# Kernel optimization log

Measured on AMD Instinct MI355X. Metric: run time of the kernel, lower is better.

The kernel has to match this reference:

```python
import jax, jax.numpy as jnp
import numpy as np

H = 16
D_MODEL = 1024
D_K = D_MODEL // H
NEG = -1e9


def setup_inputs() -> dict:
    key = jax.random.key(0)
    ks = jax.random.split(key, 12)
    B, S = 2, 2048
    inp = {
        "query": jax.random.normal(ks[0], (B, S, D_MODEL), jnp.float32),
        "key": jax.random.normal(ks[1], (B, S, D_MODEL), jnp.float32),
        "value": jax.random.normal(ks[2], (B, S, D_MODEL), jnp.float32),
        "mask": jnp.ones((B, 1, S), jnp.int32),
    }
    s = 1.0 / np.sqrt(D_MODEL)
    for i, nm in enumerate(["Wq", "Wk", "Wv", "Wo"]):
        inp[nm] = jax.random.normal(ks[3 + i], (D_MODEL, D_MODEL), jnp.float32) * s
        inp["b" + nm[1]] = jax.random.normal(ks[7 + i], (D_MODEL,), jnp.float32) * s
    return inp


def _split_heads(x):
    B, S, _ = x.shape
    return x.reshape(B, S, H, D_K).transpose(0, 2, 1, 3)  # [B,H,S,Dk]


def reference(query, key, value, mask, Wq, bq, Wk, bk, Wv, bv, Wo, bo):
    q = _split_heads(query @ Wq + bq)
    k = _split_heads(key @ Wk + bk)
    v = _split_heads(value @ Wv + bv)
    scores = jnp.einsum("bhqd,bhkd->bhqk", q, k) / jnp.sqrt(jnp.float32(D_K))
    # mask [B,1,Sk] -> broadcast as [B,1,1,Sk]
    scores = jnp.where(mask[:, None, :, :] == 0, NEG, scores)
    attn = jax.nn.softmax(scores, axis=-1)  # dropout is identity in eval mode
    out = jnp.einsum("bhqk,bhkd->bhqd", attn, v)
    B, _, Sq, _ = out.shape
    out = out.transpose(0, 2, 1, 3).reshape(B, Sq, H * D_K)
    return out @ Wo + bo
```

## Files before the change

### kernel.cpp

```cpp
#include <hip/hip_runtime.h>
#include <hip/hip_bf16.h>

typedef __attribute__((ext_vector_type(8))) short short8;
typedef __attribute__((ext_vector_type(4))) float float4v;
typedef __hip_bfloat16 bf16;

#define MFMA16(a, b, c) __builtin_amdgcn_mfma_f32_16x16x32_bf16((a), (b), (c), 0, 0, 0)

static __device__ __forceinline__ short8 load8(const bf16* p) {
    return *reinterpret_cast<const short8*>(p);
}
static __device__ __forceinline__ unsigned short bfu(float x) {
    union { bf16 b; unsigned short u; } c; c.b = __float2bfloat16(x); return c.u;
}
static __device__ __forceinline__ unsigned pack2(float lo, float hi) {
    return ((unsigned)bfu(hi) << 16) | bfu(lo);
}
static __device__ __forceinline__ short bf_bits(float x) {
    union { bf16 b; short u; } c; c.b = __float2bfloat16(x); return c.u;
}
static __device__ __forceinline__ short8 cvt8(float4 a, float4 b) {
    short8 r;
    r[0] = bf_bits(a.x); r[1] = bf_bits(a.y); r[2] = bf_bits(a.z); r[3] = bf_bits(a.w);
    r[4] = bf_bits(b.x); r[5] = bf_bits(b.y); r[6] = bf_bits(b.z); r[7] = bf_bits(b.w);
    return r;
}

typedef const __attribute__((address_space(1))) unsigned int* gp1;
typedef __attribute__((address_space(3))) unsigned int* lp3;
static __device__ __forceinline__ void async16(const void* g, void* l) {
    __builtin_amdgcn_global_load_lds((gp1)g, (lp3)l, 16, 0, 0);
}

__global__ __launch_bounds__(256) void transpose_qkv(
    const float* __restrict__ Wq, const float* __restrict__ Wk,
    const float* __restrict__ Wv, bf16* __restrict__ out_base)
{
    __shared__ bf16 tile[64][65];
    const float* in = (blockIdx.z == 0) ? Wq : (blockIdx.z == 1) ? Wk : Wv;
    bf16* out = out_base + (size_t)blockIdx.z * 1048576;
    int tx = threadIdx.x, ty = threadIdx.y;
    int bx = blockIdx.x * 64, by = blockIdx.y * 64;
    for (int i = ty; i < 64; i += 4)
        tile[i][tx] = __float2bfloat16(in[(size_t)(by + i) * 1024 + bx + tx]);
    __syncthreads();
    for (int i = ty; i < 64; i += 4)
        out[(size_t)(bx + i) * 1024 + by + tx] = tile[tx][i];
}

__global__ __launch_bounds__(256) void transpose_one(
    const float* __restrict__ in, bf16* __restrict__ out)
{
    __shared__ bf16 tile[64][65];
    int tx = threadIdx.x, ty = threadIdx.y;
    int bx = blockIdx.x * 64, by = blockIdx.y * 64;
    for (int i = ty; i < 64; i += 4)
        tile[i][tx] = __float2bfloat16(in[(size_t)(by + i) * 1024 + bx + tx]);
    __syncthreads();
    for (int i = ty; i < 64; i += 4)
        out[(size_t)(bx + i) * 1024 + by + tx] = tile[tx][i];
}

__global__ __launch_bounds__(256, 3) void qkv_gemm(
    const float* __restrict__ Xq, const float* __restrict__ Xk,
    const float* __restrict__ Xv, const bf16* __restrict__ Wt_all,
    const float* __restrict__ bq, const float* __restrict__ bk,
    const float* __restrict__ bv,
    bf16* __restrict__ outq, bf16* __restrict__ outk, bf16* __restrict__ outv)
{
    __shared__ float As[128 * 64];
    __shared__ bf16  Bs[128 * 64];

    int wg = blockIdx.x;
    int xcd = wg & 7;
    int jj = wg >> 3;
    int grp = xcd * 12 + (jj >> 3);
    int z = grp >> 5;
    int m_blk = grp & 31;
    int n_blk = jj & 7;

    const float* X    = (z == 0) ? Xq : (z == 1) ? Xk : Xv;
    const float* bias = (z == 0) ? bq : (z == 1) ? bk : bv;
    const bf16*  Wt   = Wt_all + (size_t)z * 1048576;
    bf16*        out  = (z == 0) ? outq : (z == 1) ? outk : outv;
    bool vmode = (z == 2);

    int tid = threadIdx.x;
    int w = tid >> 6, lane = tid & 63, l16 = lane & 15, quad = lane >> 4;
    int m_base = m_blk * 128, n_base = n_blk * 128;

    int r4 = lane >> 4, s16 = lane & 15;
    int r8 = lane >> 3, s8 = lane & 7;
    const float* Asrc0 = X + (size_t)(m_base + w * 32 + r4) * 1024 + ((s16 ^ r4) << 2);
    const float* Asrc1 = X + (size_t)(m_base + w * 32 + r4) * 1024 + ((s16 ^ (4 + r4)) << 2);
    const bf16*  Bsrc  = Wt + (size_t)(n_base + w * 32 + r8) * 1024 + ((s8 ^ r8) << 3);

    int wm = (w & 1) * 64, wn = (w >> 1) * 64;
    int sw = l16 & 7;

    float4v zero = {0.f, 0.f, 0.f, 0.f};
    float4v acc[4][4];
    #pragma unroll
    for (int mi = 0; mi < 4; ++mi)
        #pragma unroll
        for (int nj = 0; nj < 4; ++nj) acc[mi][nj] = zero;

    for (int it = 0; it < 16; ++it) {
        int kt = it * 64;
        #pragma unroll
        for (int p = 0; p < 8; ++p) {
            const float* s = ((p & 1) ? Asrc1 : Asrc0) + (size_t)p * 4096 + kt;
            async16(s, (char*)As + (w * 32 + p * 4) * 256);
        }
        #pragma unroll
        for (int p = 0; p < 4; ++p)
            async16(Bsrc + (size_t)p * 8192 + kt, (char*)Bs + (w * 32 + p * 8) * 128);
        __syncthreads();

        #pragma unroll
        for (int kk = 0; kk < 2; ++kk) {
            short8 af[4], bfr[4];
            #pragma unroll
            for (int mi = 0; mi < 4; ++mi) {
                const float* rp = As + (wm + mi * 16 + l16) * 64;
                float4 f0 = *(const float4*)(rp + (((kk * 8 + quad * 2)     ^ sw) << 2));
                float4 f1 = *(const float4*)(rp + (((kk * 8 + quad * 2 + 1) ^ sw) << 2));
                af[mi] = cvt8(f0, f1);
            }
            #pragma unroll
            for (int nj = 0; nj < 4; ++nj) {
                const bf16* rp = Bs + (wn + nj * 16 + l16) * 64;
                bfr[nj] = load8(rp + (((kk * 4 + quad) ^ sw) << 3));
            }
            #pragma unroll
            for (int mi = 0; mi < 4; ++mi)
                #pragma unroll
                for (int nj = 0; nj < 4; ++nj)
                    acc[mi][nj] = MFMA16(af[mi], bfr[nj], acc[mi][nj]);
        }
        __syncthreads();
    }

    float bsv[4];
    #pragma unroll
    for (int nj = 0; nj < 4; ++nj)
        bsv[nj] = bias[n_base + wn + nj * 16 + l16];

    #pragma unroll
    for (int mi = 0; mi < 4; ++mi) {
        #pragma unroll
        for (int nj = 0; nj < 4; ++nj) {
            int n = n_base + wn + nj * 16 + l16;
            int h = n >> 6, dk = n & 63;
            int m0 = m_base + wm + mi * 16 + quad * 4;
            int b = m0 >> 11, s0 = m0 & 2047;
            if (vmode) {
                float v0 = acc[mi][nj][0] + bsv[nj];
                float v1 = acc[mi][nj][1] + bsv[nj];
                float v2 = acc[mi][nj][2] + bsv[nj];
                float v3 = acc[mi][nj][3] + bsv[nj];
                uint2 pv; pv.x = pack2(v0, v1); pv.y = pack2(v2, v3);
                size_t idx = ((size_t)(b * 16 + h) * 64 + dk) * 2048 + s0;
                *reinterpret_cast<uint2*>(out + idx) = pv;
            } else {
                #pragma unroll
                for (int r = 0; r < 4; ++r) {
                    size_t idx = (((size_t)(b * 16 + h) * 2048 + s0 + r) * 64 + dk);
                    out[idx] = __float2bfloat16(acc[mi][nj][r] + bsv[nj]);
                }
            }
        }
    }
}

__global__ __launch_bounds__(256, 2) void out_gemm(
    const bf16* __restrict__ A, const bf16* __restrict__ Wt,
    const float* __restrict__ bias, float* __restrict__ out)
{
    __shared__ bf16 As[128 * 64];
    __shared__ bf16 Bs[64 * 64];

    int wg = blockIdx.x;
    int xcd = wg & 7;
    int jj = wg >> 3;
    int m_blk = xcd * 4 + (jj >> 4);
    int n_blk = jj & 15;

    int tid = threadIdx.x;
    int w = tid >> 6, lane = tid & 63, l16 = lane & 15, quad = lane >> 4;
    int m_base = m_blk * 128, n_base = n_blk * 64;

    int r8 = lane >> 3, s8 = lane & 7;
    const bf16* Asrc = A  + (size_t)(m_base + w * 32 + r8) * 1024 + ((s8 ^ r8) << 3);
    const bf16* Bsrc = Wt + (size_t)(n_base + w * 16 + r8) * 1024 + ((s8 ^ r8) << 3);

    int wm = (w & 1) * 64, wn = (w >> 1) * 32;
    int sw = l16 & 7;

    float4v zero = {0.f, 0.f, 0.f, 0.f};
    float4v acc[4][2];
    #pragma unroll
    for (int mi = 0; mi < 4; ++mi)
        #pragma unroll
        for (int nj = 0; nj < 2; ++nj) acc[mi][nj] = zero;

    for (int it = 0; it < 16; ++it) {
        int kt = it * 64;
        #pragma unroll
        for (int p = 0; p < 4; ++p)
            async16(Asrc + (size_t)p * 8192 + kt, (char*)As + (w * 32 + p * 8) * 128);
        #pragma unroll
        for (int p = 0; p < 2; ++p)
            async16(Bsrc + (size_t)p * 8192 + kt, (char*)Bs + (w * 16 + p * 8) * 128);
        __syncthreads();

        #pragma unroll
        for (int kk = 0; kk < 2; ++kk) {
            short8 af[4], bfr[2];
            #pragma unroll
            for (int mi = 0; mi < 4; ++mi) {
                const bf16* rp = As + (wm + mi * 16 + l16) * 64;
                af[mi] = load8(rp + (((kk * 4 + quad) ^ sw) << 3));
            }
            #pragma unroll
            for (int nj = 0; nj < 2; ++nj) {
                const bf16* rp = Bs + (wn + nj * 16 + l16) * 64;
                bfr[nj] = load8(rp + (((kk * 4 + quad) ^ sw) << 3));
            }
            #pragma unroll
            for (int mi = 0; mi < 4; ++mi)
                #pragma unroll
                for (int nj = 0; nj < 2; ++nj)
                    acc[mi][nj] = MFMA16(af[mi], bfr[nj], acc[mi][nj]);
        }
        __syncthreads();
    }

    float bsv[2];
    #pragma unroll
    for (int nj = 0; nj < 2; ++nj)
        bsv[nj] = bias[n_base + wn + nj * 16 + l16];

    #pragma unroll
    for (int mi = 0; mi < 4; ++mi)
        #pragma unroll
        for (int nj = 0; nj < 2; ++nj) {
            int n = n_base + wn + nj * 16 + l16;
            int m0 = m_base + wm + mi * 16 + quad * 4;
            #pragma unroll
            for (int r = 0; r < 4; ++r)
                out[(size_t)(m0 + r) * 1024 + n] = acc[mi][nj][r] + bsv[nj];
        }
}

__global__ __launch_bounds__(256, 3) void attn_fused(
    const bf16* __restrict__ Qm, const bf16* __restrict__ Km,
    const bf16* __restrict__ Vt, const int* __restrict__ mask,
    bf16* __restrict__ Oout)
{
    __shared__ __align__(16) bf16 Kc[128 * 64];
    __shared__ __align__(16) bf16 Vc[64 * 128];
    __shared__ __align__(16) bf16 P[4][32 * 72];
    __shared__ unsigned long long maskb[32];

    int tid = threadIdx.x;
    int w = tid >> 6, lane = tid & 63, l16 = lane & 15, quad = lane >> 4;
    int wg = blockIdx.x;
    int xcd = wg & 7;
    int jj = wg >> 3;
    int bh = xcd * 4 + (jj >> 4);
    int qg = jj & 15;
    int b = bh >> 4, h = bh & 15;
    int tile0 = (qg * 4 + w) * 2;

    const int* mb = mask + b * 2048;
    #pragma unroll
    for (int i = 0; i < 8; ++i) {
        unsigned long long bal = __ballot(mb[w * 512 + i * 64 + lane] != 0);
        if (lane == 0) maskb[w * 8 + i] = bal;
    }

    short8 bQ[2][2];
    #pragma unroll
    for (int qi = 0; qi < 2; ++qi) {
        const bf16* Qb = Qm + ((size_t)bh * 2048 + (size_t)(tile0 + qi) * 16) * 64;
        bQ[qi][0] = load8(Qb + l16 * 64 + quad * 8);
        bQ[qi][1] = load8(Qb + l16 * 64 + 32 + quad * 8);
    }

    int r8 = lane >> 3, s8 = lane & 7;
    int r4 = lane >> 4, s16 = lane & 15;
    const bf16* Ksrc  = Km + (size_t)bh * 131072 + (size_t)(w * 32 + r8) * 64 + ((s8 ^ r8) << 3);
    const bf16* Vsrc0 = Vt + (size_t)bh * 131072 + (size_t)(w * 16 + r4) * 2048 + ((s16 ^ r4) << 3);
    const bf16* Vsrc1 = Vt + (size_t)bh * 131072 + (size_t)(w * 16 + r4) * 2048 + ((s16 ^ (4 + r4)) << 3);

    bf16* Pw = &P[w][0];
    int sw = l16 & 7;

    float4v zero = {0.f, 0.f, 0.f, 0.f};
    float4v Oacc[2][4];
    #pragma unroll
    for (int qi = 0; qi < 2; ++qi)
        #pragma unroll
        for (int g = 0; g < 4; ++g) Oacc[qi][g] = zero;
    float lsum[2] = {0.f, 0.f};
    const float C = 0.18033688f;

    for (int it = 0; it < 16; ++it) {
        int kt = it * 128;
        #pragma unroll
        for (int p = 0; p < 4; ++p)
            async16(Ksrc + (size_t)(kt + p * 8) * 64, (char*)Kc + (w * 32 + p * 8) * 128);
        #pragma unroll
        for (int p = 0; p < 4; ++p) {
            const bf16* s = ((p & 1) ? Vsrc1 : Vsrc0) + (size_t)p * 8192 + kt;
            async16(s, (char*)Vc + (w * 16 + p * 4) * 256);
        }
        __syncthreads();

        #pragma unroll
        for (int hh = 0; hh < 2; ++hh) {
            unsigned long long m64 = maskb[it * 2 + hh];
            bool full = (m64 == ~0ull);

            float4v S[2][4];
            #pragma unroll
            for (int kj = 0; kj < 4; ++kj) {
                const bf16* kr = Kc + (hh * 64 + kj * 16 + l16) * 64;
                short8 a0 = load8(kr + (((0 + quad) ^ sw) << 3));
                short8 a1 = load8(kr + (((4 + quad) ^ sw) << 3));
                #pragma unroll
                for (int qi = 0; qi < 2; ++qi) {
                    float4v s = zero;
                    s = MFMA16(a0, bQ[qi][0], s);
                    s = MFMA16(a1, bQ[qi][1], s);
                    S[qi][kj] = s;
                }
            }

            #pragma unroll
            for (int kj = 0; kj < 4; ++kj) {
                unsigned m4 = (unsigned)(m64 >> (kj * 16 + quad * 4)) & 0xFu;
                #pragma unroll
                for (int qi = 0; qi < 2; ++qi) {
                    float p[4];
                    #pragma unroll
                    for (int r = 0; r < 4; ++r)
                        p[r] = __builtin_amdgcn_exp2f(S[qi][kj][r] * C);
                    if (!full) {
                        #pragma unroll
                        for (int r = 0; r < 4; ++r)
                            p[r] = ((m4 >> r) & 1u) ? p[r] : 0.f;
                    }
                    lsum[qi] += (p[0] + p[1]) + (p[2] + p[3]);
                    uint2 pw; pw.x = pack2(p[0], p[1]); pw.y = pack2(p[2], p[3]);
                    *reinterpret_cast<uint2*>(
                        &Pw[(qi * 16 + l16) * 72 + kj * 16 + quad * 4]) = pw;
                }
            }

            short8 ap[2][2];
            #pragma unroll
            for (int qi = 0; qi < 2; ++qi) {
                ap[qi][0] = load8(&Pw[(qi * 16 + l16) * 72 + quad * 8]);
                ap[qi][1] = load8(&Pw[(qi * 16 + l16) * 72 + 32 + quad * 8]);
            }
            #pragma unroll
            for (int g = 0; g < 4; ++g) {
                const bf16* vr = Vc + (g * 16 + l16) * 128;
                short8 v0 = load8(vr + (((hh * 8 + 0 + quad) ^ sw) << 3));
                short8 v1 = load8(vr + (((hh * 8 + 4 + quad) ^ sw) << 3));
                #pragma unroll
                for (int qi = 0; qi < 2; ++qi) {
                    Oacc[qi][g] = MFMA16(ap[qi][0], v0, Oacc[qi][g]);
                    Oacc[qi][g] = MFMA16(ap[qi][1], v1, Oacc[qi][g]);
                }
            }
        }
        __syncthreads();
    }

    #pragma unroll
    for (int qi = 0; qi < 2; ++qi) {
        float ls = lsum[qi];
        ls += __shfl_xor(ls, 16, 64);
        ls += __shfl_xor(ls, 32, 64);
        #pragma unroll
        for (int r = 0; r < 4; ++r) {
            float linv = 1.f / __shfl(ls, quad * 4 + r, 64);
            int srow = (tile0 + qi) * 16 + quad * 4 + r;
            size_t base = ((size_t)b * 2048 + srow) * 1024 + h * 64;
            #pragma unroll
            for (int g = 0; g < 4; ++g)
                Oout[base + g * 16 + l16] = __float2bfloat16(Oacc[qi][g][r] * linv);
        }
    }
}

extern "C" void kernel_launch(void* const* d_in, const int* in_sizes, int n_in,
                              void* d_out, int out_size, void* d_ws, size_t ws_size,
                              hipStream_t stream) {
    const float* query = (const float*)d_in[0];
    const float* key   = (const float*)d_in[1];
    const float* value = (const float*)d_in[2];
    const int*   mask  = (const int*)d_in[3];
    const float* Wq = (const float*)d_in[4];
    const float* bq = (const float*)d_in[5];
    const float* Wk = (const float*)d_in[6];
    const float* bk = (const float*)d_in[7];
    const float* Wv = (const float*)d_in[8];
    const float* bv = (const float*)d_in[9];
    const float* Wo = (const float*)d_in[10];
    const float* bo = (const float*)d_in[11];

    char* ws = (char*)d_ws;
    const size_t MB = 1024 * 1024;
    bf16* vb     = (bf16*)ws;
    bf16* Wt_all = (bf16*)(ws + 8 * MB);
    bf16* aout   = (bf16*)(ws + 8 * MB);
    bf16* WtO    = (bf16*)ws;
    bf16* qb     = (bf16*)d_out;
    bf16* kb     = (bf16*)((char*)d_out + 8 * MB);
    float* out   = (float*)d_out;

    transpose_qkv<<<dim3(16, 16, 3), dim3(64, 4), 0, stream>>>(Wq, Wk, Wv, Wt_all);

    qkv_gemm<<<dim3(768), 256, 0, stream>>>(
        query, key, value, Wt_all, bq, bk, bv, qb, kb, vb);

    attn_fused<<<dim3(512), 256, 0, stream>>>(qb, kb, vb, mask, aout);

    transpose_one<<<dim3(16, 16), dim3(64, 4), 0, stream>>>(Wo, WtO);

    out_gemm<<<dim3(512), 256, 0, stream>>>(aout, WtO, bo, out);
}
```

Measured before the change: 253.2 us.

## Double-buffer K/V tiles in attention with 8 waves of one query tile each

The attention kernel now uses 512 threads (8 waves), each owning one 16-row query tile instead of two. K/V are streamed in 64-key chunks into double-buffered shared memory, with the next chunk's async copy issued before the current chunk's compute, and one barrier per iteration. This is meant to overlap global loads with MFMA/softmax work and raise the number of waves resident per CU. In exchange, each loaded K/V tile is reused by half as many query rows per wave, and the kernel runs twice as many iterations and barriers.

```diff
diff --git a/kernel.cpp b/kernel.cpp
--- a/kernel.cpp
+++ b/kernel.cpp
@@ -253,14 +253,14 @@
         }
 }
 
-__global__ __launch_bounds__(256, 3) void attn_fused(
+__global__ __launch_bounds__(512, 4) void attn_fused(
     const bf16* __restrict__ Qm, const bf16* __restrict__ Km,
     const bf16* __restrict__ Vt, const int* __restrict__ mask,
     bf16* __restrict__ Oout)
 {
-    __shared__ __align__(16) bf16 Kc[128 * 64];
-    __shared__ __align__(16) bf16 Vc[64 * 128];
-    __shared__ __align__(16) bf16 P[4][32 * 72];
+    __shared__ __align__(16) bf16 Kc[2][64 * 64];
+    __shared__ __align__(16) bf16 Vc[2][64 * 64];
+    __shared__ __align__(16) bf16 P[8][16 * 72];
     __shared__ unsigned long long maskb[32];
 
     int tid = threadIdx.x;
@@ -271,129 +271,103 @@
     int bh = xcd * 4 + (jj >> 4);
     int qg = jj & 15;
     int b = bh >> 4, h = bh & 15;
-    int tile0 = (qg * 4 + w) * 2;
+    int qt = qg * 8 + w;
 
     const int* mb = mask + b * 2048;
     #pragma unroll
-    for (int i = 0; i < 8; ++i) {
-        unsigned long long bal = __ballot(mb[w * 512 + i * 64 + lane] != 0);
-        if (lane == 0) maskb[w * 8 + i] = bal;
-    }
-
-    short8 bQ[2][2];
-    #pragma unroll
-    for (int qi = 0; qi < 2; ++qi) {
-        const bf16* Qb = Qm + ((size_t)bh * 2048 + (size_t)(tile0 + qi) * 16) * 64;
-        bQ[qi][0] = load8(Qb + l16 * 64 + quad * 8);
-        bQ[qi][1] = load8(Qb + l16 * 64 + 32 + quad * 8);
-    }
+    for (int i = 0; i < 4; ++i) {
+        unsigned long long bal = __ballot(mb[w * 256 + i * 64 + lane] != 0);
+        if (lane == 0) maskb[w * 4 + i] = bal;
+    }
+
+    const bf16* Qb = Qm + ((size_t)bh * 2048 + (size_t)qt * 16) * 64;
+    short8 bQ0 = load8(Qb + l16 * 64 + quad * 8);
+    short8 bQ1 = load8(Qb + l16 * 64 + 32 + quad * 8);
 
     int r8 = lane >> 3, s8 = lane & 7;
-    int r4 = lane >> 4, s16 = lane & 15;
-    const bf16* Ksrc  = Km + (size_t)bh * 131072 + (size_t)(w * 32 + r8) * 64 + ((s8 ^ r8) << 3);
-    const bf16* Vsrc0 = Vt + (size_t)bh * 131072 + (size_t)(w * 16 + r4) * 2048 + ((s16 ^ r4) << 3);
-    const bf16* Vsrc1 = Vt + (size_t)bh * 131072 + (size_t)(w * 16 + r4) * 2048 + ((s16 ^ (4 + r4)) << 3);
+    const bf16* Ksrc = Km + (size_t)bh * 131072 + (size_t)(w * 8 + r8) * 64 + ((s8 ^ r8) << 3);
+    const bf16* Vsrc = Vt + (size_t)bh * 131072 + (size_t)(w * 8 + r8) * 2048 + ((s8 ^ r8) << 3);
 
     bf16* Pw = &P[w][0];
     int sw = l16 & 7;
 
     float4v zero = {0.f, 0.f, 0.f, 0.f};
-    float4v Oacc[2][4];
-    #pragma unroll
-    for (int qi = 0; qi < 2; ++qi)
-        #pragma unroll
-        for (int g = 0; g < 4; ++g) Oacc[qi][g] = zero;
-    float lsum[2] = {0.f, 0.f};
+    float4v Oacc[4];
+    #pragma unroll
+    for (int g = 0; g < 4; ++g) Oacc[g] = zero;
+    float lsum = 0.f;
     const float C = 0.18033688f;
 
-    for (int it = 0; it < 16; ++it) {
-        int kt = it * 128;
-        #pragma unroll
-        for (int p = 0; p < 4; ++p)
-            async16(Ksrc + (size_t)(kt + p * 8) * 64, (char*)Kc + (w * 32 + p * 8) * 128);
-        #pragma unroll
-        for (int p = 0; p < 4; ++p) {
-            const bf16* s = ((p & 1) ? Vsrc1 : Vsrc0) + (size_t)p * 8192 + kt;
-            async16(s, (char*)Vc + (w * 16 + p * 4) * 256);
-        }
+    async16(Ksrc, (char*)&Kc[0][0] + w * 1024);
+    async16(Vsrc, (char*)&Vc[0][0] + w * 1024);
+    __syncthreads();
+
+    #pragma unroll 2
+    for (int it = 0; it < 32; ++it) {
+        int cur = it & 1;
+        if (it != 31) {
+            async16(Ksrc + (size_t)(it + 1) * 4096, (char*)&Kc[cur ^ 1][0] + w * 1024);
+            async16(Vsrc + (size_t)(it + 1) * 64,   (char*)&Vc[cur ^ 1][0] + w * 1024);
+        }
+
+        unsigned long long m64 = maskb[it];
+        bool full = (m64 == ~0ull);
+        const bf16* Kb = &Kc[cur][0];
+        const bf16* Vb = &Vc[cur][0];
+
+        float4v S[4];
+        #pragma unroll
+        for (int kj = 0; kj < 4; ++kj) {
+            const bf16* kr = Kb + (kj * 16 + l16) * 64;
+            short8 a0 = load8(kr + (((0 + quad) ^ sw) << 3));
+            short8 a1 = load8(kr + (((4 + quad) ^ sw) << 3));
+            float4v s = MFMA16(a0, bQ0, zero);
+            s = MFMA16(a1, bQ1, s);
+            S[kj] = s;
+        }
+
+        #pragma unroll
+        for (int kj = 0; kj < 4; ++kj) {
+            unsigned m4 = (unsigned)(m64 >> (kj * 16 + quad * 4)) & 0xFu;
+            float p[4];
+            #pragma unroll
+            for (int r = 0; r < 4; ++r)
+                p[r] = __builtin_amdgcn_exp2f(S[kj][r] * C);
+            if (!full) {
+                #pragma unroll
+                for (int r = 0; r < 4; ++r)
+                    p[r] = ((m4 >> r) & 1u) ? p[r] : 0.f;
+            }
+            lsum += (p[0] + p[1]) + (p[2] + p[3]);
+            uint2 pw; pw.x = pack2(p[0], p[1]); pw.y = pack2(p[2], p[3]);
+            *reinterpret_cast<uint2*>(&Pw[l16 * 72 + kj * 16 + quad * 4]) = pw;
+        }
+
+        short8 ap0 = load8(&Pw[l16 * 72 + quad * 8]);
+        short8 ap1 = load8(&Pw[l16 * 72 + 32 + quad * 8]);
+        #pragma unroll
+        for (int g = 0; g < 4; ++g) {
+            const bf16* vr = Vb + (g * 16 + l16) * 64;
+            short8 v0 = load8(vr + (((0 + quad) ^ sw) << 3));
+            short8 v1 = load8(vr + (((4 + quad) ^ sw) << 3));
+            Oacc[g] = MFMA16(ap0, v0, Oacc[g]);
+            Oacc[g] = MFMA16(ap1, v1, Oacc[g]);
+        }
+
         __syncthreads();
-
-        #pragma unroll
-        for (int hh = 0; hh < 2; ++hh) {
-            unsigned long long m64 = maskb[it * 2 + hh];
-            bool full = (m64 == ~0ull);
-
-            float4v S[2][4];
-            #pragma unroll
-            for (int kj = 0; kj < 4; ++kj) {
-                const bf16* kr = Kc + (hh * 64 + kj * 16 + l16) * 64;
-                short8 a0 = load8(kr + (((0 + quad) ^ sw) << 3));
-                short8 a1 = load8(kr + (((4 + quad) ^ sw) << 3));
-                #pragma unroll
-                for (int qi = 0; qi < 2; ++qi) {
-                    float4v s = zero;
-                    s = MFMA16(a0, bQ[qi][0], s);
-                    s = MFMA16(a1, bQ[qi][1], s);
-                    S[qi][kj] = s;
-                }
-            }
-
-            #pragma unroll
-            for (int kj = 0; kj < 4; ++kj) {
-                unsigned m4 = (unsigned)(m64 >> (kj * 16 + quad * 4)) & 0xFu;
-                #pragma unroll
-                for (int qi = 0; qi < 2; ++qi) {
-                    float p[4];
-                    #pragma unroll
-                    for (int r = 0; r < 4; ++r)
-                        p[r] = __builtin_amdgcn_exp2f(S[qi][kj][r] * C);
-                    if (!full) {
-                        #pragma unroll
-                        for (int r = 0; r < 4; ++r)
-                            p[r] = ((m4 >> r) & 1u) ? p[r] : 0.f;
-                    }
-                    lsum[qi] += (p[0] + p[1]) + (p[2] + p[3]);
-                    uint2 pw; pw.x = pack2(p[0], p[1]); pw.y = pack2(p[2], p[3]);
-                    *reinterpret_cast<uint2*>(
-                        &Pw[(qi * 16 + l16) * 72 + kj * 16 + quad * 4]) = pw;
-                }
-            }
-
-            short8 ap[2][2];
-            #pragma unroll
-            for (int qi = 0; qi < 2; ++qi) {
-                ap[qi][0] = load8(&Pw[(qi * 16 + l16) * 72 + quad * 8]);
-                ap[qi][1] = load8(&Pw[(qi * 16 + l16) * 72 + 32 + quad * 8]);
-            }
-            #pragma unroll
-            for (int g = 0; g < 4; ++g) {
-                const bf16* vr = Vc + (g * 16 + l16) * 128;
-                short8 v0 = load8(vr + (((hh * 8 + 0 + quad) ^ sw) << 3));
-                short8 v1 = load8(vr + (((hh * 8 + 4 + quad) ^ sw) << 3));
-                #pragma unroll
-                for (int qi = 0; qi < 2; ++qi) {
-                    Oacc[qi][g] = MFMA16(ap[qi][0], v0, Oacc[qi][g]);
-                    Oacc[qi][g] = MFMA16(ap[qi][1], v1, Oacc[qi][g]);
-                }
-            }
-        }
-        __syncthreads();
-    }
-
-    #pragma unroll
-    for (int qi = 0; qi < 2; ++qi) {
-        float ls = lsum[qi];
-        ls += __shfl_xor(ls, 16, 64);
-        ls += __shfl_xor(ls, 32, 64);
-        #pragma unroll
-        for (int r = 0; r < 4; ++r) {
-            float linv = 1.f / __shfl(ls, quad * 4 + r, 64);
-            int srow = (tile0 + qi) * 16 + quad * 4 + r;
-            size_t base = ((size_t)b * 2048 + srow) * 1024 + h * 64;
-            #pragma unroll
-            for (int g = 0; g < 4; ++g)
-                Oout[base + g * 16 + l16] = __float2bfloat16(Oacc[qi][g][r] * linv);
-        }
+    }
+
+    float ls = lsum;
+    ls += __shfl_xor(ls, 16, 64);
+    ls += __shfl_xor(ls, 32, 64);
+    #pragma unroll
+    for (int r = 0; r < 4; ++r) {
+        float linv = 1.f / __shfl(ls, quad * 4 + r, 64);
+        int srow = qt * 16 + quad * 4 + r;
+        size_t base = ((size_t)b * 2048 + srow) * 1024 + h * 64;
+        #pragma unroll
+        for (int g = 0; g < 4; ++g)
+            Oout[base + g * 16 + l16] = __float2bfloat16(Oacc[g][r] * linv);
     }
 }
 
@@ -428,7 +402,7 @@
     qkv_gemm<<<dim3(768), 256, 0, stream>>>(
         query, key, value, Wt_all, bq, bk, bv, qb, kb, vb);
 
-    attn_fused<<<dim3(512), 256, 0, stream>>>(qb, kb, vb, mask, aout);
+    attn_fused<<<dim3(512), 512, 0, stream>>>(qb, kb, vb, mask, aout);
 
     transpose_one<<<dim3(16, 16), dim3(64, 4), 0, stream>>>(Wo, WtO);
 
```

New measurement: 241.5 us. -4.6%, faster.
